# Kernel tuning notes

Hardware: AMD Instinct MI355X
Metric: run time of the kernel (lower is better)

## Reference

```python
import jax, jax.numpy as jnp
import numpy as np

B, T, D, H = 8, 1024, 1024, 16
HD = D // H  # 64
FF = 4 * D


def setup_inputs() -> dict:
    key = jax.random.key(0)
    ks = jax.random.split(key, 16)
    s = lambda k, shape, scale: (jax.random.normal(k, shape, dtype=jnp.float32) * scale)
    return {
        "x": s(ks[0], (B, T, D), 1.0),
        "ln1_g": jnp.ones((D,), jnp.float32),
        "ln1_b": jnp.zeros((D,), jnp.float32),
        "ln2_g": jnp.ones((D,), jnp.float32),
        "ln2_b": jnp.zeros((D,), jnp.float32),
        "Wq": s(ks[1], (H, D, HD), 0.02), "bq": jnp.zeros((H, HD), jnp.float32),
        "Wk": s(ks[2], (H, D, HD), 0.02), "bk": jnp.zeros((H, HD), jnp.float32),
        "Wv": s(ks[3], (H, D, HD), 0.02), "bv": jnp.zeros((H, HD), jnp.float32),
        "Wo": s(ks[4], (D, D), 0.02), "bo": jnp.zeros((D,), jnp.float32),
        "W1": s(ks[5], (D, FF), 0.02), "b1": jnp.zeros((FF,), jnp.float32),
        "W2": s(ks[6], (FF, D), 0.02), "b2": jnp.zeros((D,), jnp.float32),
    }


def layer_norm(x, g, b, eps=1e-5):
    mu = jnp.mean(x, axis=-1, keepdims=True)
    var = jnp.mean(jnp.square(x - mu), axis=-1, keepdims=True)
    return (x - mu) * jax.lax.rsqrt(var + eps) * g + b


def reference(x, ln1_g, ln1_b, ln2_g, ln2_b, Wq, bq, Wk, bk, Wv, bv, Wo, bo, W1, b1, W2, b2):
    h = layer_norm(x, ln1_g, ln1_b)
    # Per-head Q/K/V projections, batched over heads (equivalent to the
    # Python loop of per-head Linears in the original module).
    q = jnp.einsum("btd,hde->bhte", h, Wq) + bq[None, :, None, :]
    k = jnp.einsum("btd,hde->bhte", h, Wk) + bk[None, :, None, :]
    v = jnp.einsum("btd,hde->bhte", h, Wv) + bv[None, :, None, :]
    scores = jnp.einsum("bhte,bhse->bhts", q, k) / jnp.sqrt(jnp.float32(HD))
    att = jax.nn.softmax(scores, axis=-1)  # no causal mask in source
    ctx = jnp.einsum("bhts,bhse->bhte", att, v)
    # concat heads along feature dim
    ctx = jnp.transpose(ctx, (0, 2, 1, 3)).reshape(B, T, D)
    attn_out = ctx @ Wo + bo
    x = x + attn_out
    h2 = layer_norm(x, ln2_g, ln2_b)
    ff = jax.nn.gelu(h2 @ W1 + b1, approximate=False) @ W2 + b2
    return x + ff
```

## Files before the change

### kernel.cpp

```cpp
#include <hip/hip_runtime.h>
#include <hip/hip_bf16.h>
#include <cstdint>
#include <cstddef>


typedef __bf16 bf16;
typedef __bf16 bf16x8 __attribute__((ext_vector_type(8)));
typedef __bf16 bf16x4 __attribute__((ext_vector_type(4)));
typedef float  f32x4  __attribute__((ext_vector_type(4)));

#define BB    8
#define TT    1024
#define DD    1024
#define HH    16
#define HDIM  64
#define FFD   4096
#define MROWS (BB*TT)

__device__ __forceinline__ void async_ld16(const void* g, void* l) {
  __builtin_amdgcn_global_load_lds(
      (const __attribute__((address_space(1))) uint32_t*)g,
      (__attribute__((address_space(3))) uint32_t*)l, 16, 0, 0);
}

__global__ void k_transpose_cast(const float* __restrict__ src, bf16* __restrict__ dst,
                                 int K, int N) {
  __shared__ float tile[32][33];
  const size_t boff = (size_t)blockIdx.z * K * N;
  src += boff; dst += boff;
  const int k0 = blockIdx.y * 32, n0 = blockIdx.x * 32;
  const int tx = threadIdx.x, ty = threadIdx.y;
#pragma unroll
  for (int i = 0; i < 4; ++i)
    tile[ty + i*8][tx] = src[(size_t)(k0 + ty + i*8) * N + n0 + tx];
  __syncthreads();
#pragma unroll
  for (int i = 0; i < 4; ++i)
    dst[(size_t)(n0 + ty + i*8) * K + k0 + tx] = (bf16)tile[tx][ty + i*8];
}

__global__ void k_concat_bias(const float* __restrict__ bq, const float* __restrict__ bk,
                              const float* __restrict__ bv, float* __restrict__ out) {
  int i = blockIdx.x * 256 + threadIdx.x;
  float v = (i < 1024) ? bq[i] : (i < 2048) ? bk[i - 1024] : bv[i - 2048];
  out[i] = v;
}

__global__ void k_transpose_v(const bf16* __restrict__ qkv, bf16* __restrict__ vT) {
  __shared__ bf16 tile[32][33];
  const int bh = blockIdx.z;
  const int b = bh >> 4, h = bh & 15;
  const int t0 = blockIdx.x * 32, e0 = blockIdx.y * 32;
  const int tx = threadIdx.x, ty = threadIdx.y;
  const bf16* src = qkv + (size_t)b * TT * 3072 + 2048 + h * 64;
#pragma unroll
  for (int i = 0; i < 4; ++i)
    tile[ty + i*8][tx] = src[(size_t)(t0 + ty + i*8) * 3072 + e0 + tx];
  __syncthreads();
  bf16* dst = vT + ((size_t)bh * 64 + e0) * TT + t0;
#pragma unroll
  for (int i = 0; i < 4; ++i)
    dst[(size_t)(ty + i*8) * TT + tx] = tile[tx][ty + i*8];
}

__global__ void k_layernorm(const float* __restrict__ x, const float* __restrict__ g,
                            const float* __restrict__ b, bf16* __restrict__ out) {
  const int row = blockIdx.x, tid = threadIdx.x;
  const float* xr = x + (size_t)row * DD;
  f32x4 v = *(const f32x4*)(xr + tid * 4);
  float s  = v[0] + v[1] + v[2] + v[3];
  float ss = v[0]*v[0] + v[1]*v[1] + v[2]*v[2] + v[3]*v[3];
#pragma unroll
  for (int m = 1; m < 64; m <<= 1) { s += __shfl_xor(s, m); ss += __shfl_xor(ss, m); }
  __shared__ float red[8];
  const int wid = tid >> 6;
  if ((tid & 63) == 0) { red[wid*2] = s; red[wid*2+1] = ss; }
  __syncthreads();
  s  = red[0] + red[2] + red[4] + red[6];
  ss = red[1] + red[3] + red[5] + red[7];
  const float mu = s * (1.0f / DD);
  const float var = ss * (1.0f / DD) - mu * mu;
  const float rs = rsqrtf(var + 1e-5f);
  bf16x4 o;
#pragma unroll
  for (int j = 0; j < 4; ++j)
    o[j] = (bf16)((v[j] - mu) * rs * g[tid*4 + j] + b[tid*4 + j]);
  *(bf16x4*)&out[(size_t)row * DD + tid * 4] = o;
}

template<int MODE>
__global__ __launch_bounds__(256)
void k_gemm(const bf16* __restrict__ A, const bf16* __restrict__ Bt,
            const float* __restrict__ bias, const float* __restrict__ res,
            bf16* __restrict__ outb, float* __restrict__ outf,
            int M, int N, int K) {
  __shared__ __align__(16) bf16 As[128 * 64];
  __shared__ __align__(16) bf16 Bs[128 * 64];
  const int tid = threadIdx.x;
  const int w = tid >> 6, l = tid & 63;
  const int wm = w >> 1, wn = w & 1;
  const int l15 = l & 15, l4 = l >> 4;
  const int m0 = blockIdx.y * 128, n0 = blockIdx.x * 128;

  f32x4 acc[4][4] = {};

  const int srow0 = w * 32 + (l >> 3);
  const int sl7 = l & 7;

  for (int k0 = 0; k0 < K; k0 += 64) {
#pragma unroll
    for (int j = 0; j < 4; ++j) {
      const int row = srow0 + j * 8;
      const int ch = sl7 ^ (row & 7);
      async_ld16(A + (size_t)(m0 + row) * K + k0 + ch * 8, &As[(w*32 + j*8) * 64]);
    }
#pragma unroll
    for (int j = 0; j < 4; ++j) {
      const int row = srow0 + j * 8;
      const int ch = sl7 ^ (row & 7);
      async_ld16(Bt + (size_t)(n0 + row) * K + k0 + ch * 8, &Bs[(w*32 + j*8) * 64]);
    }
    __syncthreads();
#pragma unroll
    for (int kk = 0; kk < 2; ++kk) {
      bf16x8 af[4], bfr[4];
#pragma unroll
      for (int mf = 0; mf < 4; ++mf) {
        const int row = wm*64 + mf*16 + l15;
        const int ch = (kk*4 + l4) ^ (row & 7);
        af[mf] = *(const bf16x8*)&As[row*64 + ch*8];
      }
#pragma unroll
      for (int nf = 0; nf < 4; ++nf) {
        const int row = wn*64 + nf*16 + l15;
        const int ch = (kk*4 + l4) ^ (row & 7);
        bfr[nf] = *(const bf16x8*)&Bs[row*64 + ch*8];
      }
#pragma unroll
      for (int mf = 0; mf < 4; ++mf)
#pragma unroll
        for (int nf = 0; nf < 4; ++nf)
          acc[mf][nf] = __builtin_amdgcn_mfma_f32_16x16x32_bf16(af[mf], bfr[nf], acc[mf][nf], 0, 0, 0);
    }
    __syncthreads();
  }

#pragma unroll
  for (int mf = 0; mf < 4; ++mf) {
#pragma unroll
    for (int r = 0; r < 4; ++r) {
      const size_t grow = (size_t)(m0 + wm*64 + mf*16 + l4*4 + r);
      const size_t rowoff = grow * (size_t)N;
#pragma unroll
      for (int nf = 0; nf < 4; ++nf) {
        const int gcol = n0 + wn*64 + nf*16 + l15;
        float v = acc[mf][nf][r] + bias[gcol];
        if constexpr (MODE == 1)
          v = 0.5f * v * (1.0f + erff(v * 0.70710678118654752440f));
        if constexpr (MODE == 2) {
          v += res[rowoff + gcol];
          outf[rowoff + gcol] = v;
        } else {
          outb[rowoff + gcol] = (bf16)v;
        }
      }
    }
  }
}

__global__ __launch_bounds__(256)
void k_attn(const bf16* __restrict__ qkv, const bf16* __restrict__ vT,
            bf16* __restrict__ ctx) {
  const int qt = blockIdx.x, h = blockIdx.y, b = blockIdx.z;
  const int tid = threadIdx.x;
  const int w = tid >> 6, l = tid & 63;
  const int l15 = l & 15, l4 = l >> 4;

  __shared__ __align__(16) bf16 Ks[2][64 * 64];
  __shared__ __align__(16) bf16 Vs[2][64 * 64];
  __shared__ __align__(16) bf16 P[4][16][72];

  const bf16* base = qkv + (size_t)b * TT * 3072;
  const bf16* Qp = base + h * 64;
  const bf16* Kp = base + 1024 + h * 64;
  const bf16* Vtp = vT + ((size_t)(b * HH + h)) * HDIM * TT;

  const int qrow = qt * 64 + w * 16 + l15;
  bf16x8 qf[2];
  qf[0] = *(const bf16x8*)&Qp[(size_t)qrow * 3072 + l4 * 8];
  qf[1] = *(const bf16x8*)&Qp[(size_t)qrow * 3072 + 32 + l4 * 8];

  f32x4 oacc[4] = {};
  float mrow[4] = {-1e30f, -1e30f, -1e30f, -1e30f};
  float lrow[4] = {0.f, 0.f, 0.f, 0.f};

  const int sr = (l >> 3);
  const int sl7 = l & 7;

  auto stage = [&](int buf, int t) {
    const int kv0 = t * 64;
#pragma unroll
    for (int j = 0; j < 2; ++j) {
      const int row = w*16 + j*8 + sr;
      const int ch = sl7 ^ (row & 7);
      async_ld16(Kp + (size_t)(kv0 + row) * 3072 + ch * 8, &Ks[buf][(w*16 + j*8) * 64]);
    }
#pragma unroll
    for (int j = 0; j < 2; ++j) {
      const int row = w*16 + j*8 + sr;
      const int ch = sl7 ^ (row & 7);
      async_ld16(Vtp + (size_t)row * TT + kv0 + ch * 8, &Vs[buf][(w*16 + j*8) * 64]);
    }
  };

  stage(0, 0);
  for (int t = 0; t < TT / 64; ++t) {
    const int cur = t & 1;
    __syncthreads();
    if (t + 1 < TT / 64) stage(cur ^ 1, t + 1);

    f32x4 sacc[4] = {};
#pragma unroll
    for (int nf = 0; nf < 4; ++nf) {
      const int row = nf*16 + l15;
#pragma unroll
      for (int kk = 0; kk < 2; ++kk) {
        const int ch = (kk*4 + l4) ^ (row & 7);
        bf16x8 kfr = *(const bf16x8*)&Ks[cur][row*64 + ch*8];
        sacc[nf] = __builtin_amdgcn_mfma_f32_16x16x32_bf16(qf[kk], kfr, sacc[nf], 0, 0, 0);
      }
    }
    float mnew[4], ef[4];
#pragma unroll
    for (int r = 0; r < 4; ++r) {
      float mx = -1e30f;
#pragma unroll
      for (int nf = 0; nf < 4; ++nf) { sacc[nf][r] *= 0.125f; mx = fmaxf(mx, sacc[nf][r]); }
      mx = fmaxf(mx, __shfl_xor(mx, 1));
      mx = fmaxf(mx, __shfl_xor(mx, 2));
      mx = fmaxf(mx, __shfl_xor(mx, 4));
      mx = fmaxf(mx, __shfl_xor(mx, 8));
      mnew[r] = fmaxf(mrow[r], mx);
      ef[r] = __expf(mrow[r] - mnew[r]);
      mrow[r] = mnew[r];
    }
#pragma unroll
    for (int r = 0; r < 4; ++r) {
      float rs = 0.f;
#pragma unroll
      for (int nf = 0; nf < 4; ++nf) {
        const float p = __expf(sacc[nf][r] - mnew[r]);
        rs += p;
        P[w][l4*4 + r][l15 + nf*16] = (bf16)p;
      }
      rs += __shfl_xor(rs, 1); rs += __shfl_xor(rs, 2);
      rs += __shfl_xor(rs, 4); rs += __shfl_xor(rs, 8);
      lrow[r] = lrow[r] * ef[r] + rs;
#pragma unroll
      for (int nf = 0; nf < 4; ++nf) oacc[nf][r] *= ef[r];
    }
#pragma unroll
    for (int kk = 0; kk < 2; ++kk) {
      bf16x8 pa = *(const bf16x8*)&P[w][l15][kk*32 + l4*8];
#pragma unroll
      for (int nf = 0; nf < 4; ++nf) {
        const int row = nf*16 + l15;
        const int ch = (kk*4 + l4) ^ (row & 7);
        bf16x8 vb = *(const bf16x8*)&Vs[cur][row*64 + ch*8];
        oacc[nf] = __builtin_amdgcn_mfma_f32_16x16x32_bf16(pa, vb, oacc[nf], 0, 0, 0);
      }
    }
  }
  bf16* outp = ctx + ((size_t)b * TT + qt * 64 + w * 16) * DD + h * 64;
#pragma unroll
  for (int nf = 0; nf < 4; ++nf)
#pragma unroll
    for (int r = 0; r < 4; ++r)
      outp[(size_t)(l4*4 + r) * DD + l15 + nf*16] = (bf16)(oacc[nf][r] / lrow[r]);
}

extern "C" void kernel_launch(void* const* d_in, const int* in_sizes, int n_in,
                              void* d_out, int out_size, void* d_ws, size_t ws_size,
                              hipStream_t stream) {
  const float* x     = (const float*)d_in[0];
  const float* ln1_g = (const float*)d_in[1];
  const float* ln1_b = (const float*)d_in[2];
  const float* ln2_g = (const float*)d_in[3];
  const float* ln2_b = (const float*)d_in[4];
  const float* Wq    = (const float*)d_in[5];
  const float* bq    = (const float*)d_in[6];
  const float* Wk    = (const float*)d_in[7];
  const float* bk    = (const float*)d_in[8];
  const float* Wv    = (const float*)d_in[9];
  const float* bv    = (const float*)d_in[10];
  const float* Wo    = (const float*)d_in[11];
  const float* bo    = (const float*)d_in[12];
  const float* W1    = (const float*)d_in[13];
  const float* b1    = (const float*)d_in[14];
  const float* W2    = (const float*)d_in[15];
  const float* b2    = (const float*)d_in[16];
  float* out = (float*)d_out;

  char* ws = (char*)d_ws;
  bf16* h1    = (bf16*)(ws + 0);
  bf16* vT    = (bf16*)(ws + 0);
  bf16* qkv   = (bf16*)(ws + 16777216);
  bf16* ctx   = (bf16*)(ws + 67108864);
  bf16* u     = (bf16*)(ws + 16777216);
  float* x1   = (float*)(ws + 83886080);
  bf16* wtqkv = (bf16*)(ws + 117440512);
  bf16* wot   = (bf16*)(ws + 123731968);
  bf16* w1t   = (bf16*)(ws + 125829120);
  bf16* w2t   = (bf16*)(ws + 134217728);
  float* bqkv = (float*)(ws + 142606336);
  bf16* h2 = h1;

  dim3 tb(32, 8);
  k_transpose_cast<<<dim3(2, 32, 16), tb, 0, stream>>>(Wq, wtqkv, DD, HDIM);
  k_transpose_cast<<<dim3(2, 32, 16), tb, 0, stream>>>(Wk, wtqkv + 1024*1024, DD, HDIM);
  k_transpose_cast<<<dim3(2, 32, 16), tb, 0, stream>>>(Wv, wtqkv + 2048*1024, DD, HDIM);
  k_transpose_cast<<<dim3(32, 32, 1), tb, 0, stream>>>(Wo, wot, DD, DD);
  k_transpose_cast<<<dim3(128, 32, 1), tb, 0, stream>>>(W1, w1t, DD, FFD);
  k_transpose_cast<<<dim3(32, 128, 1), tb, 0, stream>>>(W2, w2t, FFD, DD);
  k_concat_bias<<<dim3(12), 256, 0, stream>>>(bq, bk, bv, bqkv);

  k_layernorm<<<dim3(MROWS), 256, 0, stream>>>(x, ln1_g, ln1_b, h1);

  k_gemm<0><<<dim3(24, 64), 256, 0, stream>>>(h1, wtqkv, bqkv, nullptr,
                                              qkv, nullptr, MROWS, 3072, DD);

  k_transpose_v<<<dim3(32, 2, 128), tb, 0, stream>>>(qkv, vT);

  k_attn<<<dim3(16, 16, 8), 256, 0, stream>>>(qkv, vT, ctx);

  k_gemm<2><<<dim3(8, 64), 256, 0, stream>>>(ctx, wot, bo, x,
                                             nullptr, x1, MROWS, DD, DD);

  k_layernorm<<<dim3(MROWS), 256, 0, stream>>>(x1, ln2_g, ln2_b, h2);

  k_gemm<1><<<dim3(32, 64), 256, 0, stream>>>(h2, w1t, b1, nullptr,
                                              u, nullptr, MROWS, FFD, DD);

  k_gemm<2><<<dim3(8, 64), 256, 0, stream>>>(u, w2t, b2, x1,
                                             nullptr, out, MROWS, DD, FFD);

  (void)in_sizes; (void)n_in; (void)out_size; (void)ws_size;
}
```

Measured before the change: 479.5 us.

## Add 256x256 double-buffered 8-wave GEMM kernel for QKV and FFN1 projections

Adds a new GEMM kernel that uses 256x256 output tiles with 512 threads and double-buffered LDS filled by async global-to-LDS loads. It interleaves LDS staging with MFMA phases and raises wave priority during the MFMA bursts. It also remaps workgroup IDs so neighbouring tiles land on the same XCD. The kernel replaces the 128x128 GEMM for the QKV projection and the GELU FFN1 projection, aiming to raise data reuse per LDS byte and hide memory latency. The cost is 128KB of LDS per block, which limits each CU to one block, and a more fragile hand-written wait/barrier schedule.

```diff
diff --git a/kernel.cpp b/kernel.cpp
--- a/kernel.cpp
+++ b/kernel.cpp
@@ -86,6 +86,147 @@
   for (int j = 0; j < 4; ++j)
     o[j] = (bf16)((v[j] - mu) * rs * g[tid*4 + j] + b[tid*4 + j]);
   *(bf16x4*)&out[(size_t)row * DD + tid * 4] = o;
+}
+
+template<int MODE>
+__global__ __launch_bounds__(512, 2)
+void k_gemm256(const bf16* __restrict__ A, const bf16* __restrict__ Bt,
+               const float* __restrict__ bias, bf16* __restrict__ outb,
+               int M, int N, int K) {
+  __shared__ __align__(16) bf16 As[2][256 * 64];
+  __shared__ __align__(16) bf16 Bs[2][256 * 64];
+  const int tid = threadIdx.x;
+  const int w = tid >> 6, l = tid & 63;
+  const int wm = w >> 2, wn = w & 3;
+  const int l15 = l & 15, l4 = l >> 4;
+
+  const int nbx = N >> 8;
+  const int nwg = gridDim.x;
+  const int cpx = nwg >> 3;
+  const int swz = (blockIdx.x & 7) * cpx + (blockIdx.x >> 3);
+  const int m0 = (swz / nbx) << 8, n0 = (swz % nbx) << 8;
+
+  f32x4 acc[8][4] = {};
+
+  const int srow = l >> 3;
+  const int sch = l & 7;
+
+  const int NT = K >> 6;
+
+#define STAGE_A(buf, kt, rb) { \
+    const int r_ = (rb) + w*8 + srow; \
+    const int ch_ = sch ^ (r_ & 7); \
+    async_ld16(A + (size_t)(m0 + r_) * K + (kt)*64 + ch_*8, &As[buf][((rb) + w*8)*64]); }
+#define STAGE_B(buf, kt, rb) { \
+    const int r_ = (rb) + w*8 + srow; \
+    const int ch_ = sch ^ (r_ & 7); \
+    async_ld16(Bt + (size_t)(n0 + r_) * K + (kt)*64 + ch_*8, &Bs[buf][((rb) + w*8)*64]); }
+
+  STAGE_A(0, 0, 0)   STAGE_A(0, 0, 64)  STAGE_A(0, 0, 128) STAGE_A(0, 0, 192)
+  STAGE_B(0, 0, 0)   STAGE_B(0, 0, 64)  STAGE_B(0, 0, 128) STAGE_B(0, 0, 192)
+  STAGE_A(1, 1, 0)   STAGE_A(1, 1, 64)  STAGE_A(1, 1, 128) STAGE_A(1, 1, 192)
+  asm volatile("s_waitcnt vmcnt(4)" ::: "memory");
+  __builtin_amdgcn_sched_barrier(0);
+  __builtin_amdgcn_s_barrier();
+
+  for (int t = 0; t < NT; ++t) {
+    const int p = t & 1;
+    bf16x8 a0[8], b0[4], a1[8], b1[4];
+
+#pragma unroll
+    for (int mf = 0; mf < 8; ++mf) {
+      const int row = wm*128 + mf*16 + l15;
+      const int ch = l4 ^ (row & 7);
+      a0[mf] = *(const bf16x8*)&As[p][row*64 + ch*8];
+    }
+#pragma unroll
+    for (int nf = 0; nf < 4; ++nf) {
+      const int row = wn*64 + nf*16 + l15;
+      const int ch = l4 ^ (row & 7);
+      b0[nf] = *(const bf16x8*)&Bs[p][row*64 + ch*8];
+    }
+    if (t + 1 < NT) { STAGE_B(p^1, t+1, 0) STAGE_B(p^1, t+1, 64) }
+    __builtin_amdgcn_s_barrier();
+    asm volatile("s_waitcnt lgkmcnt(0)" ::: "memory");
+    __builtin_amdgcn_sched_barrier(0);
+    __builtin_amdgcn_s_setprio(1);
+#pragma unroll
+    for (int mf = 0; mf < 4; ++mf)
+#pragma unroll
+      for (int nf = 0; nf < 4; ++nf)
+        acc[mf][nf] = __builtin_amdgcn_mfma_f32_16x16x32_bf16(a0[mf], b0[nf], acc[mf][nf], 0, 0, 0);
+    __builtin_amdgcn_s_setprio(0);
+    __builtin_amdgcn_s_barrier();
+
+#pragma unroll
+    for (int mf = 0; mf < 8; ++mf) {
+      const int row = wm*128 + mf*16 + l15;
+      const int ch = (4 + l4) ^ (row & 7);
+      a1[mf] = *(const bf16x8*)&As[p][row*64 + ch*8];
+    }
+#pragma unroll
+    for (int nf = 0; nf < 4; ++nf) {
+      const int row = wn*64 + nf*16 + l15;
+      const int ch = (4 + l4) ^ (row & 7);
+      b1[nf] = *(const bf16x8*)&Bs[p][row*64 + ch*8];
+    }
+    if (t + 1 < NT) { STAGE_B(p^1, t+1, 128) STAGE_B(p^1, t+1, 192) }
+    __builtin_amdgcn_s_barrier();
+    asm volatile("s_waitcnt lgkmcnt(0)" ::: "memory");
+    __builtin_amdgcn_sched_barrier(0);
+    __builtin_amdgcn_s_setprio(1);
+#pragma unroll
+    for (int mf = 4; mf < 8; ++mf)
+#pragma unroll
+      for (int nf = 0; nf < 4; ++nf)
+        acc[mf][nf] = __builtin_amdgcn_mfma_f32_16x16x32_bf16(a0[mf], b0[nf], acc[mf][nf], 0, 0, 0);
+    __builtin_amdgcn_s_setprio(0);
+    __builtin_amdgcn_s_barrier();
+
+    if (t + 2 < NT) { STAGE_A(p, t+2, 0) STAGE_A(p, t+2, 64) }
+    __builtin_amdgcn_s_barrier();
+    __builtin_amdgcn_s_setprio(1);
+#pragma unroll
+    for (int mf = 0; mf < 4; ++mf)
+#pragma unroll
+      for (int nf = 0; nf < 4; ++nf)
+        acc[mf][nf] = __builtin_amdgcn_mfma_f32_16x16x32_bf16(a1[mf], b1[nf], acc[mf][nf], 0, 0, 0);
+    __builtin_amdgcn_s_setprio(0);
+    __builtin_amdgcn_s_barrier();
+
+    if (t + 2 < NT) { STAGE_A(p, t+2, 128) STAGE_A(p, t+2, 192) }
+    __builtin_amdgcn_s_barrier();
+    __builtin_amdgcn_s_setprio(1);
+#pragma unroll
+    for (int mf = 4; mf < 8; ++mf)
+#pragma unroll
+      for (int nf = 0; nf < 4; ++nf)
+        acc[mf][nf] = __builtin_amdgcn_mfma_f32_16x16x32_bf16(a1[mf], b1[nf], acc[mf][nf], 0, 0, 0);
+    __builtin_amdgcn_s_setprio(0);
+    if (t < NT - 2) { asm volatile("s_waitcnt vmcnt(4)" ::: "memory"); }
+    else            { asm volatile("s_waitcnt vmcnt(0)" ::: "memory"); }
+    __builtin_amdgcn_sched_barrier(0);
+    __builtin_amdgcn_s_barrier();
+  }
+#undef STAGE_A
+#undef STAGE_B
+
+#pragma unroll
+  for (int mf = 0; mf < 8; ++mf) {
+#pragma unroll
+    for (int r = 0; r < 4; ++r) {
+      const size_t grow = (size_t)(m0 + wm*128 + mf*16 + l4*4 + r);
+      const size_t rowoff = grow * (size_t)N;
+#pragma unroll
+      for (int nf = 0; nf < 4; ++nf) {
+        const int gcol = n0 + wn*64 + nf*16 + l15;
+        float v = acc[mf][nf][r] + bias[gcol];
+        if constexpr (MODE == 1)
+          v = 0.5f * v * (1.0f + erff(v * 0.70710678118654752440f));
+        outb[rowoff + gcol] = (bf16)v;
+      }
+    }
+  }
 }
 
 template<int MODE>
@@ -326,8 +467,8 @@
 
   k_layernorm<<<dim3(MROWS), 256, 0, stream>>>(x, ln1_g, ln1_b, h1);
 
-  k_gemm<0><<<dim3(24, 64), 256, 0, stream>>>(h1, wtqkv, bqkv, nullptr,
-                                              qkv, nullptr, MROWS, 3072, DD);
+  k_gemm256<0><<<dim3((MROWS/256)*(3072/256)), 512, 0, stream>>>(
+      h1, wtqkv, bqkv, qkv, MROWS, 3072, DD);
 
   k_transpose_v<<<dim3(32, 2, 128), tb, 0, stream>>>(qkv, vT);
 
@@ -338,8 +479,8 @@
 
   k_layernorm<<<dim3(MROWS), 256, 0, stream>>>(x1, ln2_g, ln2_b, h2);
 
-  k_gemm<1><<<dim3(32, 64), 256, 0, stream>>>(h2, w1t, b1, nullptr,
-                                              u, nullptr, MROWS, FFD, DD);
+  k_gemm256<1><<<dim3((MROWS/256)*(FFD/256)), 512, 0, stream>>>(
+      h2, w1t, b1, u, MROWS, FFD, DD);
 
   k_gemm<2><<<dim3(8, 64), 256, 0, stream>>>(u, w2t, b2, x1,
                                              nullptr, out, MROWS, DD, FFD);
```

Measured after the change: 472.3 us. About the same (-1.5%).
